# Kernel optimization log

Measured on AMD Instinct MI355X. Metric: run time of the kernel, lower is better.

The kernel has to match this reference:

```python
import jax, jax.numpy as jnp
import numpy as np

L = 8192            # sequence length
V = 100000          # vocab size
E = 256             # embedding dim
H = 512             # lstm hidden dim (bidirectional total)
HD = H // 2         # per-direction hidden
TAGS = 32
T = TAGS + 2        # tagset + START/STOP
START = T - 2       # START_TAG = -2
STOP = T - 1        # STOP_TAG = -1
NEG = -10000.0


def setup_inputs() -> dict:
    key = jax.random.key(0)
    ks = jax.random.split(key, 11)
    s = 0.05
    return {
        "input_words": jax.random.randint(ks[0], (L,), 0, V),
        "embed": jax.random.normal(ks[1], (V, E), dtype=jnp.float32) * s,
        "Wih_f": jax.random.normal(ks[2], (4 * HD, E), dtype=jnp.float32) * s,
        "Whh_f": jax.random.normal(ks[3], (4 * HD, HD), dtype=jnp.float32) * s,
        "b_f": jax.random.normal(ks[4], (4 * HD,), dtype=jnp.float32) * s,
        "Wih_b": jax.random.normal(ks[5], (4 * HD, E), dtype=jnp.float32) * s,
        "Whh_b": jax.random.normal(ks[6], (4 * HD, HD), dtype=jnp.float32) * s,
        "b_b": jax.random.normal(ks[7], (4 * HD,), dtype=jnp.float32) * s,
        "W_out": jax.random.normal(ks[8], (T, H), dtype=jnp.float32) * s,
        "b_out": jax.random.normal(ks[9], (T,), dtype=jnp.float32) * s,
        "transitions": jax.random.normal(ks[10], (T, T), dtype=jnp.float32),
    }


def _lstm_dir(x, Wih, Whh, b, reverse):
    # single-layer LSTM, one direction; torch gate order i, f, g, o
    def step(carry, xt):
        h, c = carry
        g = xt @ Wih.T + h @ Whh.T + b
        i, f, gg, o = jnp.split(g, 4)
        i = jax.nn.sigmoid(i)
        f = jax.nn.sigmoid(f)
        gg = jnp.tanh(gg)
        o = jax.nn.sigmoid(o)
        c = f * c + i * gg
        h = o * jnp.tanh(c)
        return (h, c), h

    init = (jnp.zeros((HD,), x.dtype), jnp.zeros((HD,), x.dtype))
    _, hs = jax.lax.scan(step, init, x, reverse=reverse)
    return hs  # (L, HD)


def _crf_marginals(feats, transitions):
    lse = jax.nn.logsumexp
    # forward algorithm: alpha_t[j] = lse_i(alpha_{t-1}[i] + trans[j,i]) + feat_t[j]
    def fstep(alpha, feat):
        new = lse(alpha[None, :] + transitions, axis=1) + feat
        return new, new

    alpha0 = jnp.full((T,), NEG, feats.dtype).at[START].set(0.0)
    alphaL, log_alpha = jax.lax.scan(fstep, alpha0, feats)  # (L, T)

    # backward algorithm, replicating repo's init: beta_L[j] = lse_i(trans[i, j])
    beta_last = lse(transitions, axis=0)

    # beta_t[j] = lse_i(beta_{t+1}[i] + feat_{t+1}[i] + trans[i, j])
    def bstep(beta, feat_next):
        new = lse((beta + feat_next)[:, None] + transitions, axis=0)
        return new, new

    _, betas = jax.lax.scan(bstep, beta_last, feats[1:], reverse=True)
    log_beta = jnp.concatenate([betas, beta_last[None]], axis=0)  # (L, T)
    return log_alpha + log_beta


def reference(input_words, embed, Wih_f, Whh_f, b_f, Wih_b, Whh_b, b_b,
              W_out, b_out, transitions):
    x = embed[input_words]                           # (L, E)
    hf = _lstm_dir(x, Wih_f, Whh_f, b_f, reverse=False)
    hb = _lstm_dir(x, Wih_b, Whh_b, b_b, reverse=True)
    lstm_out = jnp.concatenate([hf, hb], axis=-1)    # (L, H)
    feats = lstm_out @ W_out.T + b_out               # (L, T)
    score = _crf_marginals(feats, transitions)       # (L, T)
    tags = jnp.argmax(score, axis=1)                 # (L,)
    return score, tags
```

## Files before the change

kernel.cpp:

```cpp
#include <hip/hip_runtime.h>
#include <cstdint>
#include <cstddef>

#define LSEQ 8192
#define NT   34
#define NP   36
#define SCH  64
#define CCH  128
#define F_L2E 1.4426950408889634f
#define F_LN2 0.6931471805599453f

#if __has_builtin(__builtin_amdgcn_sdot4)
#define DOT4(a,b,c) __builtin_amdgcn_sdot4((a),(b),(c),false)
#else
__device__ __forceinline__ int dot4_fb(int a,int b,int c){
  c += (int)(signed char)(a & 0xff)        * (int)(signed char)(b & 0xff);
  c += (int)(signed char)((a>>8) & 0xff)   * (int)(signed char)((b>>8) & 0xff);
  c += (int)(signed char)((a>>16) & 0xff)  * (int)(signed char)((b>>16) & 0xff);
  c += (a>>24) * (b>>24);
  return c;
}
#define DOT4(a,b,c) dot4_fb((a),(b),(c))
#endif

__device__ __forceinline__ float ex2(float x){
#if __has_builtin(__builtin_amdgcn_exp2f)
  return __builtin_amdgcn_exp2f(x);
#else
  return exp2f(x);
#endif
}
__device__ __forceinline__ float lg2(float x){
#if __has_builtin(__builtin_amdgcn_logf)
  return __builtin_amdgcn_logf(x);
#else
  return __log2f(x);
#endif
}

__device__ __forceinline__ float sigf(float x){
  return __fdividef(1.f, 1.f + ex2(-F_L2E * x));
}
__device__ __forceinline__ float tanhf_fast(float x){
  return 1.f - __fdividef(2.f, ex2(2.f * F_L2E * x) + 1.f);
}

__device__ __forceinline__ void barrier_lds(){
  asm volatile("s_waitcnt lgkmcnt(0)\n\ts_barrier" ::: "memory");
}

__global__ void k_quant(const float* __restrict__ Whh_f,
                        const float* __restrict__ Whh_b,
                        int* __restrict__ Wq, float* __restrict__ fac){
  int bid = blockIdx.x;
  int dir = bid >> 10;
  int r   = bid & 1023;
  int i   = threadIdx.x;
  const float* W = (dir ? Whh_b : Whh_f) + r * 256 + i * 4;
  float w0 = W[0], w1 = W[1], w2 = W[2], w3 = W[3];
  float m = fmaxf(fmaxf(fabsf(w0), fabsf(w1)), fmaxf(fabsf(w2), fabsf(w3)));
  for (int s = 32; s; s >>= 1) m = fmaxf(m, __shfl_xor(m, s));
  float scale = (m > 0.f) ? m / 127.f : 1.f;
  float inv = __fdividef(1.f, scale);
  int q0 = (int)rintf(w0 * inv), q1 = (int)rintf(w1 * inv);
  int q2 = (int)rintf(w2 * inv), q3 = (int)rintf(w3 * inv);
  q0 = max(-127, min(127, q0)); q1 = max(-127, min(127, q1));
  q2 = max(-127, min(127, q2)); q3 = max(-127, min(127, q3));
  int p = (q0 & 255) | ((q1 & 255) << 8) | ((q2 & 255) << 16) | ((q3 & 255) << 24);
  Wq[(dir << 16) + (r << 6) + i] = p;
  if (i == 0) fac[(dir << 10) + r] = scale * (1.f / 127.f);
}

__global__ void k_gproj(const int* __restrict__ words,
                        const float* __restrict__ embed,
                        const float* __restrict__ Wih_f, const float* __restrict__ b_f,
                        const float* __restrict__ Wih_b, const float* __restrict__ b_b,
                        float* __restrict__ G_f, float* __restrict__ G_b){
  int dir = blockIdx.y;
  const float* Wih = dir ? Wih_b : Wih_f;
  const float* bb  = dir ? b_b  : b_f;
  float* G = dir ? G_b : G_f;
  int t0 = blockIdx.x * 16;
  __shared__ __align__(16) float X[16 * 256];
  for (int idx = threadIdx.x; idx < 16 * 256; idx += 256) {
    int tt = idx >> 8, e = idx & 255;
    X[idx] = embed[(size_t)words[t0 + tt] * 256 + e];
  }
  __syncthreads();
  const float4* X4 = (const float4*)X;
  for (int rb = 0; rb < 4; rb++) {
    int r = rb * 256 + threadIdx.x;
    float bv = bb[r];
    float acc[16];
#pragma unroll
    for (int tt = 0; tt < 16; tt++) acc[tt] = bv;
    const float4* W4 = (const float4*)(Wih + (size_t)r * 256);
    for (int eb = 0; eb < 64; eb++) {
      float4 w = W4[eb];
#pragma unroll
      for (int tt = 0; tt < 16; tt++) {
        float4 x = X4[tt * 64 + eb];
        acc[tt] += w.x * x.x + w.y * x.y + w.z * x.z + w.w * x.w;
      }
    }
    for (int tt = 0; tt < 16; tt++)
      G[(size_t)(t0 + tt) * 1024 + r] = acc[tt];
  }
}

__global__ __launch_bounds__(512, 2) void k_lstm(const int* __restrict__ Wq,
                                                 const float* __restrict__ fac,
                                                 const float* __restrict__ G_f,
                                                 const float* __restrict__ G_b,
                                                 float* __restrict__ hf,
                                                 float* __restrict__ hb){
  int dir = blockIdx.x;
  const int4* Wq4 = (const int4*)(Wq + (dir << 16));
  const float* facp = fac + (dir << 10);
  const float* G = dir ? G_b : G_f;
  float* hout = dir ? hb : hf;
  int tid = threadIdx.x;
  int u   = tid >> 1;
  int par = tid & 1;
  int r0  = u + par * 512;
  int r1  = r0 + 256;

  __shared__ __align__(16) int h8[2][64];

  int4 wA[16], wB[16];
#pragma unroll
  for (int i = 0; i < 16; i++) {
    wA[i] = Wq4[r0 * 16 + i];
    wB[i] = Wq4[r1 * 16 + i];
  }
  float fA = facp[r0], fB = facp[r1];
  if (tid < 64) h8[0][tid] = 0;
  float c = 0.f;

  float ga0, ga1, gb0, gb1;
  {
    int tm0 = dir ? 8191 : 0;
    int tm1 = dir ? 8190 : 1;
    const float* p0 = G + (size_t)tm0 * 1024;
    ga0 = p0[r0]; ga1 = p0[r1];
    const float* p1 = G + (size_t)tm1 * 1024;
    gb0 = p1[r0]; gb1 = p1[r1];
  }
  __syncthreads();

  auto step = [&](int t, const int* bufR, int* bufW, float& g0, float& g1) {
    float pa0, pa1;
    {
      int tn = t + 2; if (tn > 8191) tn = 8191;
      int time2 = dir ? (8191 - tn) : tn;
      const float* p = G + (size_t)time2 * 1024;
      pa0 = p[r0]; pa1 = p[r1];
    }
    int accA = 0, accB = 0;
    const int4* h84 = (const int4*)bufR;
#pragma unroll
    for (int i = 0; i < 16; ++i) {
      int4 hv = h84[i];
      accA = DOT4(wA[i].x, hv.x, accA); accA = DOT4(wA[i].y, hv.y, accA);
      accA = DOT4(wA[i].z, hv.z, accA); accA = DOT4(wA[i].w, hv.w, accA);
      accB = DOT4(wB[i].x, hv.x, accB); accB = DOT4(wB[i].y, hv.y, accB);
      accB = DOT4(wB[i].z, hv.z, accB); accB = DOT4(wB[i].w, hv.w, accB);
    }
    float vA = (float)accA * fA + g0;
    float vB = (float)accB * fB + g1;
    float rA = __shfl_xor(vA, 1);
    float rB = __shfl_xor(vB, 1);
    float gi = par ? rA : vA;
    float gf = par ? rB : vB;
    float gg = par ? vA : rA;
    float go = par ? vB : rB;
    float is = sigf(gi), fs = sigf(gf);
    float gt = tanhf_fast(gg), os = sigf(go);
    c = fs * c + is * gt;
    float h = os * tanhf_fast(c);
    if (par == 0) {
      int time = dir ? (8191 - t) : t;
      hout[(size_t)time * 256 + u] = h;
      ((signed char*)bufW)[u] = (signed char)(int)rintf(h * 127.f);
    }
    g0 = pa0; g1 = pa1;
    barrier_lds();
  };

  for (int t = 0; t < 8192; t += 2) {
    step(t,     h8[0], h8[1], ga0, ga1);
    step(t + 1, h8[1], h8[0], gb0, gb1);
  }
}

__global__ void k_feats(const float* __restrict__ hf, const float* __restrict__ hb,
                        const float* __restrict__ W_out, const float* __restrict__ b_out,
                        float* __restrict__ feats){
  int t0 = blockIdx.x * 16;
  for (int oi = threadIdx.x; oi < 16 * NT; oi += 256) {
    int tt = oi / NT;
    int tag = oi - tt * NT;
    int t = t0 + tt;
    const float4* w4 = (const float4*)(W_out + (size_t)tag * 512);
    const float4* a4 = (const float4*)(hf + (size_t)t * 256);
    const float4* c4 = (const float4*)(hb + (size_t)t * 256);
    float acc = b_out[tag];
    for (int k = 0; k < 64; k++) {
      float4 w = w4[k]; float4 h = a4[k];
      acc += w.x * h.x + w.y * h.y + w.z * h.z + w.w * h.w;
    }
    for (int k = 0; k < 64; k++) {
      float4 w = w4[64 + k]; float4 h = c4[k];
      acc += w.x * h.x + w.y * h.y + w.z * h.z + w.w * h.w;
    }
    feats[(size_t)t * NT + tag] = acc;
  }
}

__global__ __launch_bounds__(320) void k_crf_p1(const float* __restrict__ feats,
                                                const float* __restrict__ trans,
                                                float* __restrict__ Pg,
                                                float* __restrict__ rmaxG){
  int dir = blockIdx.x >> 7;
  int c   = blockIdx.x & (CCH - 1);
  int tid = threadIdx.x;
  int t0  = c * SCH;

  __shared__ __align__(16) float TRM[NT * NP];
  __shared__ float Fe[(SCH + 1) * NT];
  __shared__ __align__(16) float Pbuf[2][NT * NP];
  __shared__ float CM[NP];
  __shared__ float RMs[NT];

  for (int idx = tid; idx < NT * NT; idx += 320) {
    int j = idx / NT, k = idx - j * NT;
    float v = (dir == 0) ? trans[j * NT + k] : trans[k * NT + j];
    TRM[j * NP + k] = v * F_L2E;
  }
  for (int idx = tid; idx < (SCH + 1) * NT; idx += 320) {
    int s = idx / NT, j = idx - s * NT;
    int t = t0 + s; if (t > LSEQ - 1) t = LSEQ - 1;
    Fe[idx] = feats[(size_t)t * NT + j] * F_L2E;
  }
  for (int idx = tid; idx < NT * NP; idx += 320) {
    int k = idx / NP, i = idx - k * NP;
    Pbuf[0][idx] = (i < NT && i == k) ? 0.f : -1e30f;
  }
  if (tid < NP) CM[tid] = (tid < NT) ? 0.f : -1e30f;
  __syncthreads();
  if (tid < NT) {
    float m = -3e38f;
    for (int k = 0; k < NT; k++) m = fmaxf(m, TRM[tid * NP + k]);
    RMs[tid] = m;
  }
  __syncthreads();
  for (int idx = tid; idx < NT * NT; idx += 320) {
    int j = idx / NT, k = idx - j * NT;
    TRM[j * NP + k] -= RMs[j];
  }
  __syncthreads();

  int cur = 0;
  int j = tid / 9, g = tid - (tid / 9) * 9;
  bool act = (tid < 306);
  int i0 = 4 * g;

  for (int s = 0; s < SCH; s++) {
    int t = (dir == 0) ? (t0 + s) : (t0 + SCH - 1 - s);
    if (dir == 1 && t == LSEQ - 1) continue;
    const float* Pc = Pbuf[cur];
    float* Pn = Pbuf[cur ^ 1];
    if (act) {
      float cm0 = CM[i0], cm1 = CM[i0 + 1], cm2 = CM[i0 + 2], cm3 = CM[i0 + 3];
      float s0 = 0, s1 = 0, s2 = 0, s3 = 0;
      const float* trp = TRM + j * NP;
      const float* fep = Fe + (t + 1 - t0) * NT;
#pragma unroll
      for (int k = 0; k < NT; k++) {
        float trv = trp[k];
        if (dir == 1) trv += fep[k];
        float4 p = *(const float4*)&Pc[k * NP + i0];
        s0 += ex2(trv + p.x - cm0);
        s1 += ex2(trv + p.y - cm1);
        s2 += ex2(trv + p.z - cm2);
        s3 += ex2(trv + p.w - cm3);
      }
      float base = RMs[j] + ((dir == 0) ? Fe[(t - t0) * NT + j] : 0.f);
      float4 o;
      o.x = base + cm0 + lg2(s0);
      o.y = base + cm1 + lg2(s1);
      o.z = (i0 + 2 < NT) ? (base + cm2 + lg2(s2)) : -1e30f;
      o.w = (i0 + 3 < NT) ? (base + cm3 + lg2(s3)) : -1e30f;
      *(float4*)&Pn[j * NP + i0] = o;
    }
    __syncthreads();
    if (tid < NP) {
      float m = -3e38f;
      const float* col = Pn + tid;
      for (int k = 0; k < NT; k++) m = fmaxf(m, col[k * NP]);
      CM[tid] = m;
    }
    cur ^= 1;
    __syncthreads();
  }

  const float* Pf = Pbuf[cur];
  size_t base = (size_t)((dir << 7) + c) * (NT * NP);
  for (int idx = tid; idx < NT * NP; idx += 320)
    Pg[base + idx] = Pf[idx];
  if (tid < NT) {
    float m = -3e38f;
    for (int i = 0; i < NT; i++) m = fmaxf(m, Pf[tid * NP + i]);
    rmaxG[((dir << 7) + c) * NT + tid] = m;
  }
}

__global__ void k_crf_p2(const float* __restrict__ trans,
                         const float* __restrict__ Pg,
                         const float* __restrict__ rmaxG,
                         float* __restrict__ vIn){
  int dir = blockIdx.x;
  int lane = threadIdx.x;
  bool a = (lane < NT);
  int j = a ? lane : 0;
  __shared__ float V[NP];

  float v;
  if (dir == 0) {
    v = (lane == 32) ? 0.f : -10000.f * F_L2E;
  } else {
    float m = -3e38f;
    for (int i = 0; i < NT; i++) m = fmaxf(m, trans[i * NT + j]);
    float s = 0.f;
    for (int i = 0; i < NT; i++) s += ex2((trans[i * NT + j] - m) * F_L2E);
    v = m * F_L2E + lg2(s);
  }
  if (lane < NP) V[lane] = -1e30f;
  barrier_lds();
  if (a) V[j] = v;
  barrier_lds();
  float vm = a ? v : -3e38f;
  for (int off = 32; off; off >>= 1) vm = fmaxf(vm, __shfl_xor(vm, off));

  if (a) {
    int c0 = (dir == 0) ? 0 : (CCH - 1);
    vIn[((size_t)(dir << 7) + c0) * NP + j] = v;
  }

  for (int it = 0; it < CCH - 1; it++) {
    int c = (dir == 0) ? it : (CCH - 1 - it);
    const float* row = Pg + ((size_t)(dir << 7) + c) * (NT * NP) + j * NP;
    float rm = rmaxG[((dir << 7) + c) * NT + j];
    float m = rm + vm;
    float s = 0.f;
#pragma unroll
    for (int k = 0; k < NP; k += 4) {
      float4 p = *(const float4*)&row[k];
      s += ex2(p.x + V[k]     - m);
      s += ex2(p.y + V[k + 1] - m);
      s += ex2(p.z + V[k + 2] - m);
      s += ex2(p.w + V[k + 3] - m);
    }
    float nv = m + lg2(s);
    if (a) V[j] = nv;
    barrier_lds();
    float x = a ? nv : -3e38f;
    for (int off = 32; off; off >>= 1) x = fmaxf(x, __shfl_xor(x, off));
    vm = x;
    int cn = (dir == 0) ? (c + 1) : (c - 1);
    if (a) vIn[((size_t)(dir << 7) + cn) * NP + j] = nv;
  }
}

__global__ void k_crf_p3(const float* __restrict__ feats,
                         const float* __restrict__ trans,
                         const float* __restrict__ vIn,
                         float* __restrict__ wsA,
                         float* __restrict__ wsB){
  int dir = blockIdx.x >> 7;
  int c   = blockIdx.x & (CCH - 1);
  int lane = threadIdx.x;
  int t0 = c * SCH;
  bool a = (lane < NT);
  int j = a ? lane : 0;
  __shared__ float A[NP];
  __shared__ float U[NP];

  float trr[NT];
  float rm = -3e38f;
#pragma unroll
  for (int k = 0; k < NT; k++) {
    float vv = (dir == 0) ? trans[j * NT + k] : trans[k * NT + j];
    trr[k] = vv * F_L2E;
    rm = fmaxf(rm, trr[k]);
  }
  if (lane < NP) { A[lane] = -1e30f; U[lane] = -1e30f; }
  float v0 = vIn[((size_t)(dir << 7) + c) * NP + j];
  barrier_lds();
  if (a) A[j] = v0;
  barrier_lds();
  float am = a ? v0 : -3e38f;
  for (int off = 32; off; off >>= 1) am = fmaxf(am, __shfl_xor(am, off));

  if (dir == 0) {
    float fe = feats[(size_t)t0 * NT + j] * F_L2E;
    for (int s = 0; s < SCH; s++) {
      int t = t0 + s;
      int tn = (t + 1 < LSEQ) ? t + 1 : LSEQ - 1;
      float fe_n = feats[(size_t)tn * NT + j] * F_L2E;
      float m = rm + am;
      float ss = 0.f;
#pragma unroll
      for (int k = 0; k < NT; k++) ss += ex2(trr[k] + A[k] - m);
      float out = m + lg2(ss) + fe;
      if (a) wsA[(size_t)t * NT + j] = out * F_LN2;
      if (a) A[j] = out;
      barrier_lds();
      float x = a ? out : -3e38f;
      for (int off = 32; off; off >>= 1) x = fmaxf(x, __shfl_xor(x, off));
      am = x;
      fe = fe_n;
    }
  } else {
    float b = v0;
    int tfirst = t0 + SCH; if (tfirst > LSEQ - 1) tfirst = LSEQ - 1;
    float fe = feats[(size_t)tfirst * NT + j] * F_L2E;
    for (int s = 0; s < SCH; s++) {
      int t = t0 + SCH - 1 - s;
      float fe_n = feats[(size_t)t * NT + j] * F_L2E;
      float out;
      if (t == LSEQ - 1) {
        out = b;
      } else {
        if (a) U[j] = b + fe;
        barrier_lds();
        float um = a ? U[j] : -3e38f;
        for (int off = 32; off; off >>= 1) um = fmaxf(um, __shfl_xor(um, off));
        float m = rm + um;
        float ss = 0.f;
#pragma unroll
        for (int k = 0; k < NT; k++) ss += ex2(trr[k] + U[k] - m);
        out = m + lg2(ss);
        barrier_lds();
      }
      if (a) wsB[(size_t)t * NT + j] = out * F_LN2;
      b = out;
      fe = fe_n;
    }
  }
}

__global__ void k_finish(const float* __restrict__ wsA, const float* __restrict__ wsB,
                         float* __restrict__ out){
  int t = blockIdx.x * 256 + threadIdx.x;
  float m = -3e38f; int bi = 0;
  for (int i = 0; i < NT; i++) {
    float sc = wsA[(size_t)t * NT + i] + wsB[(size_t)t * NT + i];
    out[(size_t)t * NT + i] = sc;
    if (sc > m) { m = sc; bi = i; }
  }
  out[(size_t)LSEQ * NT + t] = (float)bi;
}

extern "C" void kernel_launch(void* const* d_in, const int* in_sizes, int n_in,
                              void* d_out, int out_size, void* d_ws, size_t ws_size,
                              hipStream_t stream) {
  const int*   words  = (const int*)  d_in[0];
  const float* embed  = (const float*)d_in[1];
  const float* Wih_f  = (const float*)d_in[2];
  const float* Whh_f  = (const float*)d_in[3];
  const float* b_f    = (const float*)d_in[4];
  const float* Wih_b  = (const float*)d_in[5];
  const float* Whh_b  = (const float*)d_in[6];
  const float* b_b    = (const float*)d_in[7];
  const float* W_out  = (const float*)d_in[8];
  const float* b_out  = (const float*)d_in[9];
  const float* trans  = (const float*)d_in[10];
  float* out = (float*)d_out;

  float* wsf = (float*)d_ws;
  size_t off = 0;
  float* G_f   = wsf + off; off += (size_t)LSEQ * 1024;
  float* G_b   = wsf + off; off += (size_t)LSEQ * 1024;
  float* hf    = wsf + off; off += (size_t)LSEQ * 256;
  float* hb    = wsf + off; off += (size_t)LSEQ * 256;
  float* feats = wsf + off; off += (size_t)LSEQ * NT + 16;
  float* wsA   = wsf + off; off += (size_t)LSEQ * NT + 16;
  float* wsB   = wsf + off; off += (size_t)LSEQ * NT + 16;
  float* fac   = wsf + off; off += 2048;
  int*   Wq    = (int*)(wsf + off); off += 2 * 1024 * 64;
  float* Pg    = G_f;
  float* rmaxG = G_f + 256 * (NT * NP);
  float* vIn   = rmaxG + 256 * NT + 32;

  k_quant<<<2048, 64, 0, stream>>>(Whh_f, Whh_b, Wq, fac);
  k_gproj<<<dim3(512, 2), 256, 0, stream>>>(words, embed, Wih_f, b_f, Wih_b, b_b, G_f, G_b);
  k_lstm<<<2, 512, 0, stream>>>(Wq, fac, G_f, G_b, hf, hb);
  k_feats<<<512, 256, 0, stream>>>(hf, hb, W_out, b_out, feats);
  k_crf_p1<<<256, 320, 0, stream>>>(feats, trans, Pg, rmaxG);
  k_crf_p2<<<2, 64, 0, stream>>>(trans, Pg, rmaxG, vIn);
  k_crf_p3<<<256, 64, 0, stream>>>(feats, trans, vIn, wsA, wsB);
  k_finish<<<32, 256, 0, stream>>>(wsA, wsB, out);
}
```

Before: 9.263 ms.

## Broadcast LSTM hidden state via readlane and deepen input-gate prefetch to four steps

Each step of the recurrent LSTM kernel now does a single LDS load per lane of the int8 hidden vector, then broadcasts each packed word with readlane into scalar operands for the dot4 products. Before, every thread read all 16 int4 vectors from LDS. The input-projection prefetch distance also grows from two to four timesteps, with the loop unrolled by four. The aim is to cut LDS traffic and latency on the serial critical path and to hide global-load latency better. The cost is 64 readlanes per step and more register pressure.

```diff
diff --git a/kernel.cpp b/kernel.cpp
--- a/kernel.cpp
+++ b/kernel.cpp
@@ -108,66 +108,72 @@
   }
 }
 
-__global__ __launch_bounds__(512, 2) void k_lstm(const int* __restrict__ Wq,
-                                                 const float* __restrict__ fac,
-                                                 const float* __restrict__ G_f,
-                                                 const float* __restrict__ G_b,
-                                                 float* __restrict__ hf,
-                                                 float* __restrict__ hb){
+__global__
+__attribute__((amdgpu_flat_work_group_size(512, 512), amdgpu_waves_per_eu(2, 2)))
+void k_lstm(const int* __restrict__ Wq,
+            const float* __restrict__ fac,
+            const float* __restrict__ G_f,
+            const float* __restrict__ G_b,
+            float* __restrict__ hf,
+            float* __restrict__ hb){
   int dir = blockIdx.x;
   const int4* Wq4 = (const int4*)(Wq + (dir << 16));
   const float* facp = fac + (dir << 10);
   const float* G = dir ? G_b : G_f;
   float* hout = dir ? hb : hf;
-  int tid = threadIdx.x;
-  int u   = tid >> 1;
-  int par = tid & 1;
-  int r0  = u + par * 512;
-  int r1  = r0 + 256;
+  int tid  = threadIdx.x;
+  int lane = tid & 63;
+  int u    = tid >> 1;
+  int par  = tid & 1;
+  int r0   = u + par * 512;
+  int r1   = r0 + 256;
 
   __shared__ __align__(16) int h8[2][64];
 
-  int4 wA[16], wB[16];
+  int wAr[64], wBr[64];
 #pragma unroll
   for (int i = 0; i < 16; i++) {
-    wA[i] = Wq4[r0 * 16 + i];
-    wB[i] = Wq4[r1 * 16 + i];
+    int4 va = Wq4[r0 * 16 + i];
+    int4 vb = Wq4[r1 * 16 + i];
+    wAr[4*i+0] = va.x; wAr[4*i+1] = va.y; wAr[4*i+2] = va.z; wAr[4*i+3] = va.w;
+    wBr[4*i+0] = vb.x; wBr[4*i+1] = vb.y; wBr[4*i+2] = vb.z; wBr[4*i+3] = vb.w;
   }
   float fA = facp[r0], fB = facp[r1];
   if (tid < 64) h8[0][tid] = 0;
   float c = 0.f;
 
-  float ga0, ga1, gb0, gb1;
+  float ga0, ga1, gb0, gb1, gc0, gc1, gd0, gd1;
   {
     int tm0 = dir ? 8191 : 0;
     int tm1 = dir ? 8190 : 1;
-    const float* p0 = G + (size_t)tm0 * 1024;
-    ga0 = p0[r0]; ga1 = p0[r1];
-    const float* p1 = G + (size_t)tm1 * 1024;
-    gb0 = p1[r0]; gb1 = p1[r1];
+    int tm2 = dir ? 8189 : 2;
+    int tm3 = dir ? 8188 : 3;
+    const float* p;
+    p = G + (size_t)tm0 * 1024; ga0 = p[r0]; ga1 = p[r1];
+    p = G + (size_t)tm1 * 1024; gb0 = p[r0]; gb1 = p[r1];
+    p = G + (size_t)tm2 * 1024; gc0 = p[r0]; gc1 = p[r1];
+    p = G + (size_t)tm3 * 1024; gd0 = p[r0]; gd1 = p[r1];
   }
   __syncthreads();
 
   auto step = [&](int t, const int* bufR, int* bufW, float& g0, float& g1) {
-    float pa0, pa1;
+    float cur0 = g0, cur1 = g1;
     {
-      int tn = t + 2; if (tn > 8191) tn = 8191;
+      int tn = t + 4; if (tn > 8191) tn = 8191;
       int time2 = dir ? (8191 - tn) : tn;
       const float* p = G + (size_t)time2 * 1024;
-      pa0 = p[r0]; pa1 = p[r1];
-    }
+      g0 = p[r0]; g1 = p[r1];
+    }
+    int hv = bufR[lane];
     int accA = 0, accB = 0;
-    const int4* h84 = (const int4*)bufR;
-#pragma unroll
-    for (int i = 0; i < 16; ++i) {
-      int4 hv = h84[i];
-      accA = DOT4(wA[i].x, hv.x, accA); accA = DOT4(wA[i].y, hv.y, accA);
-      accA = DOT4(wA[i].z, hv.z, accA); accA = DOT4(wA[i].w, hv.w, accA);
-      accB = DOT4(wB[i].x, hv.x, accB); accB = DOT4(wB[i].y, hv.y, accB);
-      accB = DOT4(wB[i].z, hv.z, accB); accB = DOT4(wB[i].w, hv.w, accB);
-    }
-    float vA = (float)accA * fA + g0;
-    float vB = (float)accB * fB + g1;
+#pragma unroll
+    for (int j = 0; j < 64; j++) {
+      int hs = __builtin_amdgcn_readlane(hv, j);
+      accA = DOT4(wAr[j], hs, accA);
+      accB = DOT4(wBr[j], hs, accB);
+    }
+    float vA = (float)accA * fA + cur0;
+    float vB = (float)accB * fB + cur1;
     float rA = __shfl_xor(vA, 1);
     float rB = __shfl_xor(vB, 1);
     float gi = par ? rA : vA;
@@ -183,13 +189,14 @@
       hout[(size_t)time * 256 + u] = h;
       ((signed char*)bufW)[u] = (signed char)(int)rintf(h * 127.f);
     }
-    g0 = pa0; g1 = pa1;
     barrier_lds();
   };
 
-  for (int t = 0; t < 8192; t += 2) {
+  for (int t = 0; t < 8192; t += 4) {
     step(t,     h8[0], h8[1], ga0, ga1);
     step(t + 1, h8[1], h8[0], gb0, gb1);
+    step(t + 2, h8[0], h8[1], gc0, gc1);
+    step(t + 3, h8[1], h8[0], gd0, gd1);
   }
 }
 
```

Result: slower. 11.59 ms (+25.1%).

## Restructure LSTM recurrence with k-split DPP reduction and async LDS staging of gates

Applied to the files above, without the earlier changes.

The input-gate matrix G is stored interleaved as [t][unit][4 gates], so one float4 read gives all four gates of a unit. In the LSTM kernel each group of four lanes splits the 256-wide int8 dot product, and the partial sums are combined with DPP quad reductions. Each thread then holds all four gates, which removes the earlier cross-lane shuffle between gate pairs. G rows for four timesteps at a time are prefetched into double-buffered LDS with global_load_lds, taking the per-step global loads off the serial critical path. This costs extra redundant gate math per lane, a larger LDS footprint, and a vmcnt wait every fourth step.

```diff
diff --git a/kernel.cpp b/kernel.cpp
--- a/kernel.cpp
+++ b/kernel.cpp
@@ -23,6 +23,12 @@
 #define DOT4(a,b,c) dot4_fb((a),(b),(c))
 #endif
 
+#if __has_builtin(__builtin_amdgcn_global_load_lds)
+#define HAS_GLL 1
+#else
+#define HAS_GLL 0
+#endif
+
 __device__ __forceinline__ float ex2(float x){
 #if __has_builtin(__builtin_amdgcn_exp2f)
   return __builtin_amdgcn_exp2f(x);
@@ -43,6 +49,17 @@
 }
 __device__ __forceinline__ float tanhf_fast(float x){
   return 1.f - __fdividef(2.f, ex2(2.f * F_L2E * x) + 1.f);
+}
+
+__device__ __forceinline__ int qreduce(int x){
+#if __has_builtin(__builtin_amdgcn_mov_dpp)
+  x += __builtin_amdgcn_mov_dpp(x, 0xB1, 0xF, 0xF, true);
+  x += __builtin_amdgcn_mov_dpp(x, 0x4E, 0xF, 0xF, true);
+#else
+  x += __shfl_xor(x, 1);
+  x += __shfl_xor(x, 2);
+#endif
+  return x;
 }
 
 __device__ __forceinline__ void barrier_lds(){
@@ -104,7 +121,7 @@
       }
     }
     for (int tt = 0; tt < 16; tt++)
-      G[(size_t)(t0 + tt) * 1024 + r] = acc[tt];
+      G[(size_t)(t0 + tt) * 1024 + (threadIdx.x << 2) + rb] = acc[tt];
   }
 }
 
@@ -115,81 +132,114 @@
                                                  float* __restrict__ hf,
                                                  float* __restrict__ hb){
   int dir = blockIdx.x;
-  const int4* Wq4 = (const int4*)(Wq + (dir << 16));
+  const int* Wqd = Wq + (dir << 16);
   const float* facp = fac + (dir << 10);
   const float* G = dir ? G_b : G_f;
   float* hout = dir ? hb : hf;
   int tid = threadIdx.x;
-  int u   = tid >> 1;
-  int par = tid & 1;
-  int r0  = u + par * 512;
-  int r1  = r0 + 256;
-
+  int ln  = tid & 63;
+  int wv  = tid >> 6;
+  int q   = tid >> 2;
+  int kq  = tid & 3;
+  int u   = (q << 1) + (tid & 1);
+
+  __shared__ __align__(16) float GL[2][4 * 1024];
   __shared__ __align__(16) int h8[2][64];
 
-  int4 wA[16], wB[16];
-#pragma unroll
-  for (int i = 0; i < 16; i++) {
-    wA[i] = Wq4[r0 * 16 + i];
-    wB[i] = Wq4[r1 * 16 + i];
-  }
-  float fA = facp[r0], fB = facp[r1];
+  int4 w4[8][4];
+#pragma unroll
+  for (int g = 0; g < 4; g++) {
+#pragma unroll
+    for (int uu = 0; uu < 2; uu++) {
+      int r = (q << 1) + uu + (g << 8);
+      const int4* p = (const int4*)(Wqd + (r << 6) + (kq << 4));
+      w4[g * 2 + uu][0] = p[0]; w4[g * 2 + uu][1] = p[1];
+      w4[g * 2 + uu][2] = p[2]; w4[g * 2 + uu][3] = p[3];
+    }
+  }
+  float fI = facp[u], fF = facp[u + 256], fG = facp[u + 512], fO = facp[u + 768];
   if (tid < 64) h8[0][tid] = 0;
   float c = 0.f;
 
-  float ga0, ga1, gb0, gb1;
-  {
-    int tm0 = dir ? 8191 : 0;
-    int tm1 = dir ? 8190 : 1;
-    const float* p0 = G + (size_t)tm0 * 1024;
-    ga0 = p0[r0]; ga1 = p0[r1];
-    const float* p1 = G + (size_t)tm1 * 1024;
-    gb0 = p1[r0]; gb1 = p1[r1];
-  }
-  __syncthreads();
-
-  auto step = [&](int t, const int* bufR, int* bufW, float& g0, float& g1) {
-    float pa0, pa1;
-    {
-      int tn = t + 2; if (tn > 8191) tn = 8191;
-      int time2 = dir ? (8191 - tn) : tn;
-      const float* p = G + (size_t)time2 * 1024;
-      pa0 = p[r0]; pa1 = p[r1];
-    }
-    int accA = 0, accB = 0;
-    const int4* h84 = (const int4*)bufR;
-#pragma unroll
-    for (int i = 0; i < 16; ++i) {
-      int4 hv = h84[i];
-      accA = DOT4(wA[i].x, hv.x, accA); accA = DOT4(wA[i].y, hv.y, accA);
-      accA = DOT4(wA[i].z, hv.z, accA); accA = DOT4(wA[i].w, hv.w, accA);
-      accB = DOT4(wB[i].x, hv.x, accB); accB = DOT4(wB[i].y, hv.y, accB);
-      accB = DOT4(wB[i].z, hv.z, accB); accB = DOT4(wB[i].w, hv.w, accB);
-    }
-    float vA = (float)accA * fA + g0;
-    float vB = (float)accB * fB + g1;
-    float rA = __shfl_xor(vA, 1);
-    float rB = __shfl_xor(vB, 1);
-    float gi = par ? rA : vA;
-    float gf = par ? rB : vB;
-    float gg = par ? vA : rA;
-    float go = par ? vB : rB;
-    float is = sigf(gi), fs = sigf(gf);
-    float gt = tanhf_fast(gg), os = sigf(go);
+  auto stage = [&](int cn) {
+    int half = cn & 1;
+    int gt0 = dir ? (8191 - (cn * 4 + 3)) : (cn * 4);
+    const char* src = (const char*)(G + (size_t)gt0 * 1024) + (wv << 11) + (ln << 4);
+    char* dst = (char*)&GL[half][0] + (wv << 11);
+#pragma unroll
+    for (int i = 0; i < 2; i++) {
+#if HAS_GLL
+      __builtin_amdgcn_global_load_lds(
+          (const __attribute__((address_space(1))) unsigned int*)(src + (i << 10)),
+          (__attribute__((address_space(3))) unsigned int*)(dst + (i << 10)),
+          16, 0, 0);
+#else
+      *(float4*)(dst + (i << 10) + (ln << 4)) = *(const float4*)(src + (i << 10));
+#endif
+    }
+  };
+
+  auto step = [&](int t, const float* Grow, const int* bufR, int* bufW) {
+    const int4* hs = (const int4*)((const char*)bufR + (kq << 6));
+    int4 h0 = hs[0], h1 = hs[1], h2 = hs[2], h3 = hs[3];
+    int acc[8];
+#pragma unroll
+    for (int m = 0; m < 8; m++) {
+      int a = 0;
+      a = DOT4(w4[m][0].x, h0.x, a); a = DOT4(w4[m][0].y, h0.y, a);
+      a = DOT4(w4[m][0].z, h0.z, a); a = DOT4(w4[m][0].w, h0.w, a);
+      a = DOT4(w4[m][1].x, h1.x, a); a = DOT4(w4[m][1].y, h1.y, a);
+      a = DOT4(w4[m][1].z, h1.z, a); a = DOT4(w4[m][1].w, h1.w, a);
+      a = DOT4(w4[m][2].x, h2.x, a); a = DOT4(w4[m][2].y, h2.y, a);
+      a = DOT4(w4[m][2].z, h2.z, a); a = DOT4(w4[m][2].w, h2.w, a);
+      a = DOT4(w4[m][3].x, h3.x, a); a = DOT4(w4[m][3].y, h3.y, a);
+      a = DOT4(w4[m][3].z, h3.z, a); a = DOT4(w4[m][3].w, h3.w, a);
+      acc[m] = a;
+    }
+#pragma unroll
+    for (int m = 0; m < 8; m++) acc[m] = qreduce(acc[m]);
+    int p = tid & 1;
+    int aI = p ? acc[1] : acc[0];
+    int aF = p ? acc[3] : acc[2];
+    int aG = p ? acc[5] : acc[4];
+    int aO = p ? acc[7] : acc[6];
+    float4 gv = ((const float4*)Grow)[u];
+    float ri = (float)aI * fI + gv.x;
+    float rf = (float)aF * fF + gv.y;
+    float rg = (float)aG * fG + gv.z;
+    float ro = (float)aO * fO + gv.w;
+    float is = sigf(ri), fs = sigf(rf);
+    float gt = tanhf_fast(rg), os = sigf(ro);
     c = fs * c + is * gt;
     float h = os * tanhf_fast(c);
-    if (par == 0) {
+    if ((tid & 3) < 2) {
       int time = dir ? (8191 - t) : t;
       hout[(size_t)time * 256 + u] = h;
       ((signed char*)bufW)[u] = (signed char)(int)rintf(h * 127.f);
     }
-    g0 = pa0; g1 = pa1;
-    barrier_lds();
   };
 
-  for (int t = 0; t < 8192; t += 2) {
-    step(t,     h8[0], h8[1], ga0, ga1);
-    step(t + 1, h8[1], h8[0], gb0, gb1);
+  stage(0);
+  asm volatile("s_waitcnt vmcnt(0)" ::: "memory");
+  __syncthreads();
+
+  for (int cn = 0; cn < 2048; ++cn) {
+    if (cn + 1 < 2048) stage(cn + 1);
+    const float* Hc = GL[cn & 1];
+    int tb = cn << 2;
+#pragma unroll
+    for (int s = 0; s < 4; ++s) {
+      int row = dir ? (3 - s) : s;
+      const float* Grow = Hc + (row << 10);
+      int t = tb + s;
+      if ((s & 1) == 0) step(t, Grow, h8[0], h8[1]);
+      else              step(t, Grow, h8[1], h8[0]);
+      if (s == 3) {
+        asm volatile("s_waitcnt vmcnt(0) lgkmcnt(0)\n\ts_barrier" ::: "memory");
+      } else {
+        barrier_lds();
+      }
+    }
   }
 }
 
```

After: 9.454 ms. 1.02x slower.
